# Kernel optimization log

Hardware: AMD Instinct MI355X
Metric: run time of the kernel (lower is better)

Reference implementation:

```python
import jax, jax.numpy as jnp
import numpy as np

HEADS = 56
OUT = 32       # hidden_channels (per-head out dim)
N_FEAT = 128
N_CLASS = 2
N_NODES = 20000
N_EDGES = 100000
N_GRAPHS = 50
EPS_BN = 1e-5


def _gat_conv(x, W, att_src, att_dst, bias, src, dst, n, concat):
    # x: [n, in]; W: [in, H*O]; att_*: [H, O]
    h = (x @ W).reshape(n, HEADS, OUT)                     # [n, H, O]
    a_s = jnp.sum(h * att_src, axis=-1)                    # [n, H]
    a_d = jnp.sum(h * att_dst, axis=-1)                    # [n, H]
    e = jax.nn.leaky_relu(a_s[src] + a_d[dst], 0.2)        # [E, H]
    m = jax.ops.segment_max(e, dst, num_segments=n)        # per-dst max
    ex = jnp.exp(e - m[dst])
    den = jax.ops.segment_sum(ex, dst, num_segments=n)
    alpha = ex / den[dst]                                  # segment softmax over incoming edges
    msg = h[src] * alpha[:, :, None]                       # [E, H, O]
    out = jax.ops.segment_sum(msg, dst, num_segments=n)    # [n, H, O]
    if concat:
        return out.reshape(n, HEADS * OUT) + bias
    return out.mean(axis=1) + bias


def _bn_eval(x, gamma, beta, mean, var):
    return (x - mean) * jax.lax.rsqrt(var + EPS_BN) * gamma + beta


def setup_inputs() -> dict:
    key = jax.random.key(0)
    ks = jax.random.split(key, 20)
    d1 = HEADS * OUT
    inp = {
        'x': jax.random.normal(ks[0], (N_NODES, N_FEAT), jnp.float32),
        'edge_index': jax.random.randint(ks[1], (2, N_EDGES), 0, N_NODES, jnp.int32),
        'batch': jnp.sort(jax.random.randint(ks[2], (N_NODES,), 0, N_GRAPHS, jnp.int32)),
        'W1': jax.random.normal(ks[3], (N_FEAT, d1), jnp.float32) * (1.0 / np.sqrt(N_FEAT)),
        'att_src1': jax.random.normal(ks[4], (HEADS, OUT), jnp.float32) * 0.1,
        'att_dst1': jax.random.normal(ks[5], (HEADS, OUT), jnp.float32) * 0.1,
        'b1': jnp.zeros((d1,), jnp.float32),
        'bn1_g': jnp.ones((d1,), jnp.float32),
        'bn1_b': jnp.zeros((d1,), jnp.float32),
        'bn1_m': jax.random.normal(ks[6], (d1,), jnp.float32) * 0.1,
        'bn1_v': jax.random.uniform(ks[7], (d1,), jnp.float32) + 0.5,
        'W2': jax.random.normal(ks[8], (d1, d1), jnp.float32) * (1.0 / np.sqrt(d1)),
        'att_src2': jax.random.normal(ks[9], (HEADS, OUT), jnp.float32) * 0.1,
        'att_dst2': jax.random.normal(ks[10], (HEADS, OUT), jnp.float32) * 0.1,
        'b2': jnp.zeros((OUT,), jnp.float32),
        'bn2_g': jnp.ones((OUT,), jnp.float32),
        'bn2_b': jnp.zeros((OUT,), jnp.float32),
        'bn2_m': jax.random.normal(ks[11], (OUT,), jnp.float32) * 0.1,
        'bn2_v': jax.random.uniform(ks[12], (OUT,), jnp.float32) + 0.5,
        'lin_w': jax.random.normal(ks[13], (OUT, N_CLASS), jnp.float32) * (1.0 / np.sqrt(OUT)),
        'lin_b': jnp.zeros((N_CLASS,), jnp.float32),
    }
    return inp


def reference(x, edge_index, batch, W1, att_src1, att_dst1, b1, bn1_g, bn1_b, bn1_m, bn1_v,
              W2, att_src2, att_dst2, b2, bn2_g, bn2_b, bn2_m, bn2_v, lin_w, lin_b):
    n = x.shape[0]
    loop = jnp.arange(n, dtype=edge_index.dtype)
    src = jnp.concatenate([edge_index[0], loop])   # PyG GATConv add_self_loops=True
    dst = jnp.concatenate([edge_index[1], loop])

    h = jax.nn.elu(_gat_conv(x, W1, att_src1, att_dst1, b1, src, dst, n, concat=True))
    h = _bn_eval(h, bn1_g, bn1_b, bn1_m, bn1_v)
    # dropout p=0.5 is identity in eval
    h = _gat_conv(h, W2, att_src2, att_dst2, b2, src, dst, n, concat=False)
    h = _bn_eval(h, bn2_g, bn2_b, bn2_m, bn2_v)

    sums = jax.ops.segment_sum(h, batch, num_segments=N_GRAPHS)
    cnt = jax.ops.segment_sum(jnp.ones((n, 1), h.dtype), batch, num_segments=N_GRAPHS)
    pooled = sums / jnp.maximum(cnt, 1.0)          # global_mean_pool
    return pooled @ lin_w + lin_b
```

## Files before the change

kernel.cpp:

```cpp
#include <hip/hip_runtime.h>
#include <hip/hip_bf16.h>
#include <hip/hip_fp8.h>
#include <cstdint>
#include <cstddef>

#define NN     20000
#define NF     128
#define NH     56
#define OC     32
#define DD1    1792
#define NE     100000
#define ETOT   120000
#define NG     50
#define EPS_BN 1e-5f
#define GRP    16
#define EB     16

typedef __bf16 bf16x8 __attribute__((ext_vector_type(8)));
typedef float  floatx4 __attribute__((ext_vector_type(4)));
typedef float  floatx2 __attribute__((ext_vector_type(2)));
typedef unsigned int u32;
typedef __attribute__((address_space(1))) u32 gu32;
typedef __attribute__((address_space(3))) u32 lu32;

__device__ __forceinline__ void async_copy16(void* lds, const void* g) {
    __builtin_amdgcn_global_load_lds((gu32*)const_cast<void*>(g), (lu32*)lds, 16, 0, 0);
}

__device__ __forceinline__ void dec_fp8x4(u32 u, float* v) {
#if __has_builtin(__builtin_amdgcn_cvt_pk_f32_fp8)
    floatx2 lo = __builtin_amdgcn_cvt_pk_f32_fp8(u, false);
    floatx2 hi = __builtin_amdgcn_cvt_pk_f32_fp8(u, true);
    v[0] = lo[0]; v[1] = lo[1]; v[2] = hi[0]; v[3] = hi[1];
#else
    #pragma unroll
    for (int b = 0; b < 4; ++b) {
        __hip_fp8_e4m3 t;
        t.__x = (u >> (8 * b)) & 0xff;
        v[b] = (float)t;
    }
#endif
}

__device__ __forceinline__ void fma_fp8x4(u32 u, float a, float* acc) {
    float v[4];
    dec_fp8x4(u, v);
    #pragma unroll
    for (int b = 0; b < 4; ++b) acc[b] += a * v[b];
}

__global__ __launch_bounds__(256) void cast_bf16_kernel(const float* __restrict__ in,
                                                        __hip_bfloat16* __restrict__ out, int n) {
    int i = blockIdx.x * 256 + threadIdx.x;
    if (i < n) out[i] = __float2bfloat16(in[i]);
}

__global__ __launch_bounds__(256) void transpose_cast_kernel(const float* __restrict__ in,
                                                             __hip_bfloat16* __restrict__ out,
                                                             int R, int C) {
    __shared__ float tile[32][33];
    int c0 = blockIdx.x * 32, r0 = blockIdx.y * 32;
    int tx = threadIdx.x & 31, ty = threadIdx.x >> 5;
    #pragma unroll
    for (int i = 0; i < 32; i += 8) {
        int r = r0 + ty + i, c = c0 + tx;
        if (r < R && c < C) tile[ty + i][tx] = in[(size_t)r * C + c];
    }
    __syncthreads();
    #pragma unroll
    for (int i = 0; i < 32; i += 8) {
        int c = c0 + ty + i, r = r0 + tx;
        if (c < C && r < R) out[(size_t)c * R + r] = __float2bfloat16(tile[tx][ty + i]);
    }
}

__global__ __launch_bounds__(256) void hist_kernel(const int* __restrict__ ei, int* __restrict__ deg) {
    int i = blockIdx.x * 256 + threadIdx.x;
    if (i >= ETOT) return;
    int dst = (i < NE) ? ei[NE + i] : (i - NE);
    atomicAdd(&deg[dst], 1);
}

__global__ __launch_bounds__(1024) void scan_kernel(const int* __restrict__ deg,
                                                    int* __restrict__ rowptr,
                                                    int* __restrict__ cursor) {
    __shared__ int buf[1024];
    int t = threadIdx.x;
    const int CH = (NN + 1023) >> 10;
    int base = t * CH;
    int s = 0;
    for (int j = 0; j < CH; ++j) { int idx = base + j; if (idx < NN) s += deg[idx]; }
    buf[t] = s;
    __syncthreads();
    for (int off = 1; off < 1024; off <<= 1) {
        int v = (t >= off) ? buf[t - off] : 0;
        __syncthreads();
        buf[t] += v;
        __syncthreads();
    }
    int run = buf[t] - s;
    for (int j = 0; j < CH; ++j) {
        int idx = base + j;
        if (idx < NN) { rowptr[idx] = run; cursor[idx] = run; run += deg[idx]; }
    }
    if (t == 1023) rowptr[NN] = buf[1023];
}

__global__ __launch_bounds__(256) void scatter_kernel(const int* __restrict__ ei,
                                                      int* __restrict__ cursor,
                                                      int* __restrict__ csr_src) {
    int i = blockIdx.x * 256 + threadIdx.x;
    if (i >= ETOT) return;
    int s, d;
    if (i < NE) { s = ei[i]; d = ei[NE + i]; } else { s = i - NE; d = i - NE; }
    int pos = atomicAdd(&cursor[d], 1);
    csr_src[pos] = s;
}

__global__ __launch_bounds__(512, 2) void gemm_192(const __hip_bfloat16* __restrict__ A,
                                                   const __hip_bfloat16* __restrict__ Bt,
                                                   unsigned char* __restrict__ C8,
                                                   int M, int N, int K) {
    __shared__ __align__(16) unsigned short lds[2][28672];
    const int tid  = threadIdx.x;
    const int lane = tid & 63, wave = tid >> 6;
    const int wm = wave >> 2, wn = wave & 3;

    const int nbx = N >> 8;
    const int nby = (M + 191) / 192;
    const int nwg = nbx * nby;
    const int q = nwg >> 3, r = nwg & 7;
    const int xcd = blockIdx.x & 7, bidx = blockIdx.x >> 3;
    const int wg = (xcd < r ? xcd * (q + 1) : r * (q + 1) + (xcd - r) * q) + bidx;
    const int by = wg / nbx, bx = wg - by * nbx;
    const int m0 = by * 192, n0 = bx << 8;

    const int NT = K >> 6;

    const int qq = lane >> 4, rr = lane & 15;

    auto stageA = [&](int kt, int b) {
        #pragma unroll
        for (int i = 0; i < 3; ++i) {
            int slot = i * 512 + tid;
            int row = slot >> 3, pch = slot & 7;
            int lc = pch ^ (row & 7);
            int gr = m0 + row; if (gr > M - 1) gr = M - 1;
            async_copy16(&lds[b][slot * 8], A + (size_t)gr * K + (kt << 6) + lc * 8);
        }
    };
    auto stageB = [&](int kt, int b) {
        #pragma unroll
        for (int i = 0; i < 4; ++i) {
            int slot = i * 512 + tid;
            int row = slot >> 3, pch = slot & 7;
            int lc = pch ^ (row & 7);
            async_copy16(&lds[b][12288 + slot * 8], Bt + (size_t)(n0 + row) * K + (kt << 6) + lc * 8);
        }
    };

    floatx4 zero = {0.f, 0.f, 0.f, 0.f};
    floatx4 acc[6][4];
    #pragma unroll
    for (int i = 0; i < 6; ++i)
        #pragma unroll
        for (int jj = 0; jj < 4; ++jj) acc[i][jj] = zero;

    bf16x8 aF[3][2], bA[2][2], bB[2][2];

    auto loadA = [&](int b, int mg) {
        #pragma unroll
        for (int mf = 0; mf < 3; ++mf)
            #pragma unroll
            for (int s = 0; s < 2; ++s) {
                int row = wm * 96 + mg * 48 + mf * 16 + rr;
                int pch = (s * 4 + qq) ^ (row & 7);
                aF[mf][s] = *(const bf16x8*)&lds[b][row * 64 + pch * 8];
            }
    };
    auto loadB = [&](int b, bf16x8 (&bF)[2][2], int ng) {
        #pragma unroll
        for (int nf = 0; nf < 2; ++nf)
            #pragma unroll
            for (int s = 0; s < 2; ++s) {
                int row = wn * 64 + (ng * 2 + nf) * 16 + rr;
                int pch = (s * 4 + qq) ^ (row & 7);
                bF[nf][s] = *(const bf16x8*)&lds[b][12288 + row * 64 + pch * 8];
            }
    };
    auto mfmaQ = [&](int mg, int ng, bf16x8 (&bF)[2][2]) {
        #pragma unroll
        for (int mf = 0; mf < 3; ++mf)
            #pragma unroll
            for (int nf = 0; nf < 2; ++nf)
                #pragma unroll
                for (int s = 0; s < 2; ++s)
                    acc[mg * 3 + mf][ng * 2 + nf] = __builtin_amdgcn_mfma_f32_16x16x32_bf16(
                        aF[mf][s], bF[nf][s], acc[mg * 3 + mf][ng * 2 + nf], 0, 0, 0);
    };

#define SB0 __builtin_amdgcn_sched_barrier(0)
#define GBAR do { SB0; __builtin_amdgcn_s_barrier(); SB0; } while (0)

    stageB(0, 0); stageA(0, 0);
    stageB(1, 1); stageA(1, 1);
    SB0;
    asm volatile("s_waitcnt vmcnt(7)" ::: "memory");
    GBAR;

    for (int t = 0; t < NT; ++t) {
        const int p = t & 1;
        int tp = t + 2; while (tp >= NT) tp -= 2;

        loadA(p, 0); loadB(p, bA, 0);
        GBAR;
        __builtin_amdgcn_s_setprio(1);
        mfmaQ(0, 0, bA);
        __builtin_amdgcn_s_setprio(0);
        GBAR;

        loadB(p, bB, 1);
        stageB(tp, p);
        GBAR;
        __builtin_amdgcn_s_setprio(1);
        mfmaQ(0, 1, bB);
        __builtin_amdgcn_s_setprio(0);
        GBAR;

        loadA(p, 1);
        stageA(tp, p);
        SB0;
        asm volatile("s_waitcnt vmcnt(7)" ::: "memory");
        GBAR;
        __builtin_amdgcn_s_setprio(1);
        mfmaQ(1, 1, bB);
        mfmaQ(1, 0, bA);
        __builtin_amdgcn_s_setprio(0);
        GBAR;
    }
#undef GBAR
#undef SB0

    #pragma unroll
    for (int mt = 0; mt < 6; ++mt) {
        #pragma unroll
        for (int r4 = 0; r4 < 4; ++r4) {
            int rowc = m0 + wm * 96 + mt * 16 + (lane >> 4) * 4 + r4;
            if (rowc < M) {
                float v0 = acc[mt][0][r4], v1 = acc[mt][1][r4];
                float v2 = acc[mt][2][r4], v3 = acc[mt][3][r4];
                unsigned char q8[4];
#if __has_builtin(__builtin_amdgcn_cvt_pk_fp8_f32)
                u32 p01 = (u32)__builtin_amdgcn_cvt_pk_fp8_f32(v0, v1, 0, false);
                u32 p23 = (u32)__builtin_amdgcn_cvt_pk_fp8_f32(v2, v3, 0, false);
                q8[0] = p01 & 0xff; q8[1] = (p01 >> 8) & 0xff;
                q8[2] = p23 & 0xff; q8[3] = (p23 >> 8) & 0xff;
#else
                { __hip_fp8_e4m3 t0(v0), t1(v1), t2(v2), t3(v3);
                  q8[0] = t0.__x; q8[1] = t1.__x; q8[2] = t2.__x; q8[3] = t3.__x; }
#endif
                #pragma unroll
                for (int nt = 0; nt < 4; ++nt) {
                    int col = n0 + wn * 64 + nt * 16 + (lane & 15);
                    C8[(size_t)rowc * N + col] = q8[nt];
                }
            }
        }
    }
}

__global__ __launch_bounds__(256) void attn_score(const unsigned char* __restrict__ h8,
                                                  const float* __restrict__ att_src,
                                                  const float* __restrict__ att_dst,
                                                  float* __restrict__ as_,
                                                  float* __restrict__ ad_) {
    int wave = threadIdx.x >> 6, lane = threadIdx.x & 63;
    int node = blockIdx.x * 4 + wave;
    if (node >= NN || lane >= NH) return;
    const uint2* hp = (const uint2*)(h8 + (size_t)node * DD1 + lane * OC);
    float s = 0.f, d = 0.f;
    #pragma unroll
    for (int jj = 0; jj < 4; ++jj) {
        uint2 u2 = hp[jj];
        u32 us[2] = {u2.x, u2.y};
        #pragma unroll
        for (int w = 0; w < 2; ++w) {
            float v[4];
            dec_fp8x4(us[w], v);
            #pragma unroll
            for (int b = 0; b < 4; ++b) {
                int o = jj * 8 + w * 4 + b;
                s += v[b] * att_src[lane * OC + o];
                d += v[b] * att_dst[lane * OC + o];
            }
        }
    }
    as_[(size_t)node * NH + lane] = s;
    ad_[(size_t)node * NH + lane] = d;
}

template <int LAYER>
__device__ __forceinline__ void flush_node(float* acc, float den, int cur, int f, int lane,
                                           const float* __restrict__ bias,
                                           const float* __restrict__ bng,
                                           const float* __restrict__ bnb,
                                           const float* __restrict__ bnm,
                                           const float* __restrict__ bnv,
                                           void* __restrict__ outp) {
    float inv = 1.f / den;
    #pragma unroll
    for (int k = 0; k < 4; ++k) acc[k] *= inv;

    if constexpr (LAYER == 1) {
        int d0 = f * 256 + lane * 4;
        u32 r01, r23;
        {
            float v0 = acc[0] + bias[d0 + 0];
            float v1 = acc[1] + bias[d0 + 1];
            float v2 = acc[2] + bias[d0 + 2];
            float v3 = acc[3] + bias[d0 + 3];
            v0 = v0 > 0.f ? v0 : expm1f(v0);
            v1 = v1 > 0.f ? v1 : expm1f(v1);
            v2 = v2 > 0.f ? v2 : expm1f(v2);
            v3 = v3 > 0.f ? v3 : expm1f(v3);
            v0 = (v0 - bnm[d0 + 0]) * rsqrtf(bnv[d0 + 0] + EPS_BN) * bng[d0 + 0] + bnb[d0 + 0];
            v1 = (v1 - bnm[d0 + 1]) * rsqrtf(bnv[d0 + 1] + EPS_BN) * bng[d0 + 1] + bnb[d0 + 1];
            v2 = (v2 - bnm[d0 + 2]) * rsqrtf(bnv[d0 + 2] + EPS_BN) * bng[d0 + 2] + bnb[d0 + 2];
            v3 = (v3 - bnm[d0 + 3]) * rsqrtf(bnv[d0 + 3] + EPS_BN) * bng[d0 + 3] + bnb[d0 + 3];
            __hip_bfloat16 b0 = __float2bfloat16(v0), b1 = __float2bfloat16(v1);
            __hip_bfloat16 b2 = __float2bfloat16(v2), b3 = __float2bfloat16(v3);
            r01 = (u32)*(unsigned short*)&b0 | ((u32)*(unsigned short*)&b1 << 16);
            r23 = (u32)*(unsigned short*)&b2 | ((u32)*(unsigned short*)&b3 << 16);
        }
        uint2 pk; pk.x = r01; pk.y = r23;
        *(uint2*)((__hip_bfloat16*)outp + (size_t)cur * DD1 + d0) = pk;
    } else {
        #pragma unroll
        for (int k = 0; k < 4; ++k) {
            acc[k] += __shfl_xor(acc[k], 8, 64);
            acc[k] += __shfl_xor(acc[k], 16, 64);
            acc[k] += __shfl_xor(acc[k], 32, 64);
        }
        if (lane < 8) {
            floatx4 pk;
            #pragma unroll
            for (int k = 0; k < 4; ++k) pk[k] = acc[k] * (1.f / NH);
            *(floatx4*)((float*)outp + ((size_t)cur * 7 + f) * OC + lane * 4) = pk;
        }
    }
    acc[0] = acc[1] = acc[2] = acc[3] = 0.f;
}

template <int LAYER>
__global__ __launch_bounds__(256) void attn_aggregate(const int* __restrict__ rowptr,
                                                      const int* __restrict__ csr_src,
                                                      const float* __restrict__ as_,
                                                      const float* __restrict__ ad_,
                                                      const unsigned char* __restrict__ h8,
                                                      const float* __restrict__ bias,
                                                      const float* __restrict__ bng,
                                                      const float* __restrict__ bnb,
                                                      const float* __restrict__ bnm,
                                                      const float* __restrict__ bnv,
                                                      void* __restrict__ outp) {
    const int wv = threadIdx.x >> 6, lane = threadIdx.x & 63;
    const int w = blockIdx.x * 4 + wv;
    const int NWAVES = 7 * (NN / GRP);
    if (w >= NWAVES) return;
    const int f  = w % 7;
    const int g  = w / 7;
    const int n0 = g * GRP;
    const int off  = f * 256 + lane * 4;
    const int head = f * 8 + (lane >> 3);

    const int e0 = rowptr[n0], e1 = rowptr[n0 + GRP];
    int cur = n0;
    int bound = rowptr[n0 + 1];
    float adv = ad_[(size_t)cur * NH + head];

    float acc[4] = {0.f, 0.f, 0.f, 0.f};
    float m = -1e30f, den = 0.f;

    for (int e = e0; e < e1; e += EB) {
        u32   hv[EB];
        float sv[EB];
        #pragma unroll
        for (int i = 0; i < EB; ++i) {
            int idx = (e + i < e1) ? e + i : e1 - 1;
            int s = csr_src[idx];
            hv[i] = *(const u32*)(h8 + (size_t)s * DD1 + off);
            sv[i] = as_[(size_t)s * NH + head];
        }
        #pragma unroll
        for (int i = 0; i < EB; ++i) {
            if (e + i >= e1) break;
            if (e + i >= bound) {
                flush_node<LAYER>(acc, den, cur, f, lane, bias, bng, bnb, bnm, bnv, outp);
                ++cur;
                bound = rowptr[cur + 1];
                adv = ad_[(size_t)cur * NH + head];
                m = -1e30f; den = 0.f;
            }
            float lr = sv[i] + adv;
            lr = lr > 0.f ? lr : 0.2f * lr;
            float wgt;
            if (lr > m) {
                float scale = __expf(m - lr);
                den = den * scale + 1.f;
                #pragma unroll
                for (int k = 0; k < 4; ++k) acc[k] *= scale;
                m = lr;
                wgt = 1.f;
            } else {
                wgt = __expf(lr - m);
                den += wgt;
            }
            fma_fp8x4(hv[i], wgt, acc);
        }
    }
    flush_node<LAYER>(acc, den, cur, f, lane, bias, bng, bnb, bnm, bnv, outp);
}

__global__ __launch_bounds__(256) void pool_kernel(const float* __restrict__ h2part,
                                                   const int* __restrict__ batch,
                                                   float* __restrict__ sums,
                                                   float* __restrict__ cnt) {
    __shared__ float red[4][OC];
    const int g = blockIdx.x >> 3, c = blockIdx.x & 7;
    const int t = threadIdx.x;
    const int ch = t & 31, nl = t >> 5;
    int lo = 0, hi = NN;
    while (lo < hi) { int mid = (lo + hi) >> 1; if (batch[mid] < g) lo = mid + 1; else hi = mid; }
    const int s = lo;
    hi = NN;
    while (lo < hi) { int mid = (lo + hi) >> 1; if (batch[mid] <= g) lo = mid + 1; else hi = mid; }
    const int e = lo;
    const int len = e - s;
    const int n0 = s + (len * c) / 8;
    const int n1 = s + (len * (c + 1)) / 8;
    float acc = 0.f;
    for (int n = n0 + nl; n < n1; n += 8) {
        const float* p = h2part + (size_t)n * 7 * OC + ch;
        float a = 0.f;
        #pragma unroll
        for (int f = 0; f < 7; ++f) a += p[f * OC];
        acc += a;
    }
    acc += __shfl_xor(acc, 32, 64);
    if ((t & 32) == 0) red[t >> 6][ch] = acc;
    __syncthreads();
    if (t < OC) {
        float total = red[0][t] + red[1][t] + red[2][t] + red[3][t];
        atomicAdd(&sums[g * OC + t], total);
    }
    if (t == 0 && c == 0) cnt[g] = (float)len;
}

__global__ __launch_bounds__(128) void final_kernel(const float* __restrict__ sums,
                                                    const float* __restrict__ cnt,
                                                    const float* __restrict__ b2,
                                                    const float* __restrict__ bn2g,
                                                    const float* __restrict__ bn2b,
                                                    const float* __restrict__ bn2m,
                                                    const float* __restrict__ bn2v,
                                                    const float* __restrict__ lin_w,
                                                    const float* __restrict__ lin_b,
                                                    float* __restrict__ out) {
    int t = threadIdx.x;
    if (t >= NG * 2) return;
    int g = t >> 1, c = t & 1;
    float invc = 1.f / fmaxf(cnt[g], 1.f);
    float acc = lin_b[c];
    #pragma unroll
    for (int o = 0; o < OC; ++o) {
        float pooled = sums[g * OC + o] * invc + b2[o];
        float v = (pooled - bn2m[o]) * rsqrtf(bn2v[o] + EPS_BN) * bn2g[o] + bn2b[o];
        acc += v * lin_w[o * 2 + c];
    }
    out[t] = acc;
}

extern "C" void kernel_launch(void* const* d_in, const int* in_sizes, int n_in,
                              void* d_out, int out_size, void* d_ws, size_t ws_size,
                              hipStream_t stream) {
    const float* x    = (const float*)d_in[0];
    const int*   ei   = (const int*)d_in[1];
    const int*   bat  = (const int*)d_in[2];
    const float* W1   = (const float*)d_in[3];
    const float* at_s1 = (const float*)d_in[4];
    const float* at_d1 = (const float*)d_in[5];
    const float* b1   = (const float*)d_in[6];
    const float* bn1g = (const float*)d_in[7];
    const float* bn1b = (const float*)d_in[8];
    const float* bn1m = (const float*)d_in[9];
    const float* bn1v = (const float*)d_in[10];
    const float* W2   = (const float*)d_in[11];
    const float* at_s2 = (const float*)d_in[12];
    const float* at_d2 = (const float*)d_in[13];
    const float* b2   = (const float*)d_in[14];
    const float* bn2g = (const float*)d_in[15];
    const float* bn2b = (const float*)d_in[16];
    const float* bn2m = (const float*)d_in[17];
    const float* bn2v = (const float*)d_in[18];
    const float* linw = (const float*)d_in[19];
    const float* linb = (const float*)d_in[20];
    float* out = (float*)d_out;

    char* wsp = (char*)d_ws;
    auto alloc = [&](size_t bytes) -> void* {
        void* p = (void*)wsp;
        wsp += (bytes + 255) & ~(size_t)255;
        return p;
    };
    unsigned char*  h8  = (unsigned char*)alloc((size_t)NN * DD1);
    __hip_bfloat16* h1p = (__hip_bfloat16*)alloc((size_t)NN * DD1 * 2);
    __hip_bfloat16* xb  = (__hip_bfloat16*)alloc((size_t)NN * NF * 2);
    __hip_bfloat16* w1t = (__hip_bfloat16*)alloc((size_t)DD1 * NF * 2);
    __hip_bfloat16* w2t = (__hip_bfloat16*)alloc((size_t)DD1 * DD1 * 2);
    float* asb   = (float*)alloc((size_t)NN * NH * 4);
    float* adb   = (float*)alloc((size_t)NN * NH * 4);
    int*   deg   = (int*)alloc((size_t)NN * 4);
    int*   rowp  = (int*)alloc((size_t)(NN + 1) * 4);
    int*   curs  = (int*)alloc((size_t)NN * 4);
    int*   csr   = (int*)alloc((size_t)ETOT * 4);
    float* h2part = (float*)alloc((size_t)NN * 7 * OC * 4);
    float* sums  = (float*)alloc((size_t)(NG * OC + NG) * 4);
    float* cnt   = sums + NG * OC;

    hipMemsetAsync(deg, 0, (size_t)NN * 4, stream);
    hipMemsetAsync(sums, 0, (size_t)(NG * OC + NG) * 4, stream);

    cast_bf16_kernel<<<(NN * NF + 255) / 256, 256, 0, stream>>>(x, xb, NN * NF);
    transpose_cast_kernel<<<dim3(DD1 / 32, NF / 32), 256, 0, stream>>>(W1, w1t, NF, DD1);
    transpose_cast_kernel<<<dim3(DD1 / 32, DD1 / 32), 256, 0, stream>>>(W2, w2t, DD1, DD1);
    hist_kernel<<<(ETOT + 255) / 256, 256, 0, stream>>>(ei, deg);
    scan_kernel<<<1, 1024, 0, stream>>>(deg, rowp, curs);
    scatter_kernel<<<(ETOT + 255) / 256, 256, 0, stream>>>(ei, curs, csr);

    const int AGG_BLOCKS = (7 * (NN / GRP) + 3) / 4;
    const int NBY192 = (NN + 191) / 192;
    const int GEMM_BLOCKS = NBY192 * (DD1 / 256);

    gemm_192<<<GEMM_BLOCKS, 512, 0, stream>>>(xb, w1t, h8, NN, DD1, NF);
    attn_score<<<NN / 4, 256, 0, stream>>>(h8, at_s1, at_d1, asb, adb);
    attn_aggregate<1><<<AGG_BLOCKS, 256, 0, stream>>>(rowp, csr, asb, adb, h8, b1, bn1g, bn1b, bn1m, bn1v, (void*)h1p);

    gemm_192<<<GEMM_BLOCKS, 512, 0, stream>>>(h1p, w2t, h8, NN, DD1, DD1);
    attn_score<<<NN / 4, 256, 0, stream>>>(h8, at_s2, at_d2, asb, adb);
    attn_aggregate<2><<<AGG_BLOCKS, 256, 0, stream>>>(rowp, csr, asb, adb, h8, b2, bn2g, bn2b, bn2m, bn2v, (void*)h2part);

    pool_kernel<<<NG * 8, 256, 0, stream>>>(h2part, bat, sums, cnt);
    final_kernel<<<1, 128, 0, stream>>>(sums, cnt, b2, bn2g, bn2b, bn2m, bn2v, linw, linb, out);
}
```

Baseline: 575.3 us.

## Pack source attention scores beside fp8 features and remap aggregate blocks per XCD

The fp8 feature rows are padded to a 2048-byte stride. Each 256-column chunk gets a 32-byte tail that holds the 8 per-head source attention scores, so the gather in aggregation fetches the features and the score from the same row region. The separate as_ buffer goes away. The aggregate kernel also remaps block IDs so that consecutive logical blocks land on the same XCD, which should improve L2 locality for neighbouring node groups. The cost is a larger h8 buffer and strided GEMM stores.

```diff
diff --git a/kernel.cpp b/kernel.cpp
--- a/kernel.cpp
+++ b/kernel.cpp
@@ -15,6 +15,7 @@
 #define EPS_BN 1e-5f
 #define GRP    16
 #define EB     16
+#define PKROW  2048
 
 typedef __bf16 bf16x8 __attribute__((ext_vector_type(8)));
 typedef float  floatx4 __attribute__((ext_vector_type(4)));
@@ -261,23 +262,23 @@
 #endif
                 #pragma unroll
                 for (int nt = 0; nt < 4; ++nt) {
-                    int col = n0 + wn * 64 + nt * 16 + (lane & 15);
-                    C8[(size_t)rowc * N + col] = q8[nt];
+                    int inner = wn * 64 + nt * 16 + (lane & 15);
+                    C8[(size_t)rowc * PKROW + bx * 288 + inner] = q8[nt];
                 }
             }
         }
     }
 }
 
-__global__ __launch_bounds__(256) void attn_score(const unsigned char* __restrict__ h8,
+__global__ __launch_bounds__(256) void attn_score(unsigned char* __restrict__ h8,
                                                   const float* __restrict__ att_src,
                                                   const float* __restrict__ att_dst,
-                                                  float* __restrict__ as_,
                                                   float* __restrict__ ad_) {
     int wave = threadIdx.x >> 6, lane = threadIdx.x & 63;
     int node = blockIdx.x * 4 + wave;
     if (node >= NN || lane >= NH) return;
-    const uint2* hp = (const uint2*)(h8 + (size_t)node * DD1 + lane * OC);
+    const int f = lane >> 3, j = lane & 7;
+    const uint2* hp = (const uint2*)(h8 + (size_t)node * PKROW + f * 288 + j * 32);
     float s = 0.f, d = 0.f;
     #pragma unroll
     for (int jj = 0; jj < 4; ++jj) {
@@ -295,7 +296,7 @@
             }
         }
     }
-    as_[(size_t)node * NH + lane] = s;
+    *(float*)(h8 + (size_t)node * PKROW + f * 288 + 256 + j * 4) = s;
     ad_[(size_t)node * NH + lane] = d;
 }
 
@@ -354,7 +355,6 @@
 template <int LAYER>
 __global__ __launch_bounds__(256) void attn_aggregate(const int* __restrict__ rowptr,
                                                       const int* __restrict__ csr_src,
-                                                      const float* __restrict__ as_,
                                                       const float* __restrict__ ad_,
                                                       const unsigned char* __restrict__ h8,
                                                       const float* __restrict__ bias,
@@ -362,15 +362,21 @@
                                                       const float* __restrict__ bnb,
                                                       const float* __restrict__ bnm,
                                                       const float* __restrict__ bnv,
-                                                      void* __restrict__ outp) {
+                                                      void* __restrict__ outp,
+                                                      int nblocks) {
+    const int q = nblocks >> 3, r = nblocks & 7;
+    const int xcd = blockIdx.x & 7, bidx = blockIdx.x >> 3;
+    const int bid = (xcd < r ? xcd * (q + 1) : r * (q + 1) + (xcd - r) * q) + bidx;
+
     const int wv = threadIdx.x >> 6, lane = threadIdx.x & 63;
-    const int w = blockIdx.x * 4 + wv;
+    const int w = bid * 4 + wv;
     const int NWAVES = 7 * (NN / GRP);
     if (w >= NWAVES) return;
     const int f  = w % 7;
     const int g  = w / 7;
     const int n0 = g * GRP;
-    const int off  = f * 256 + lane * 4;
+    const int hoff = f * 288 + lane * 4;
+    const int soff = f * 288 + 256 + (lane >> 3) * 4;
     const int head = f * 8 + (lane >> 3);
 
     const int e0 = rowptr[n0], e1 = rowptr[n0 + GRP];
@@ -388,8 +394,9 @@
         for (int i = 0; i < EB; ++i) {
             int idx = (e + i < e1) ? e + i : e1 - 1;
             int s = csr_src[idx];
-            hv[i] = *(const u32*)(h8 + (size_t)s * DD1 + off);
-            sv[i] = as_[(size_t)s * NH + head];
+            const unsigned char* row = h8 + (size_t)s * PKROW;
+            hv[i] = *(const u32*)(row + hoff);
+            sv[i] = *(const float*)(row + soff);
         }
         #pragma unroll
         for (int i = 0; i < EB; ++i) {
@@ -512,12 +519,11 @@
         wsp += (bytes + 255) & ~(size_t)255;
         return p;
     };
-    unsigned char*  h8  = (unsigned char*)alloc((size_t)NN * DD1);
+    unsigned char*  h8  = (unsigned char*)alloc((size_t)NN * PKROW);
     __hip_bfloat16* h1p = (__hip_bfloat16*)alloc((size_t)NN * DD1 * 2);
     __hip_bfloat16* xb  = (__hip_bfloat16*)alloc((size_t)NN * NF * 2);
     __hip_bfloat16* w1t = (__hip_bfloat16*)alloc((size_t)DD1 * NF * 2);
     __hip_bfloat16* w2t = (__hip_bfloat16*)alloc((size_t)DD1 * DD1 * 2);
-    float* asb   = (float*)alloc((size_t)NN * NH * 4);
     float* adb   = (float*)alloc((size_t)NN * NH * 4);
     int*   deg   = (int*)alloc((size_t)NN * 4);
     int*   rowp  = (int*)alloc((size_t)(NN + 1) * 4);
@@ -542,12 +548,12 @@
     const int GEMM_BLOCKS = NBY192 * (DD1 / 256);
 
     gemm_192<<<GEMM_BLOCKS, 512, 0, stream>>>(xb, w1t, h8, NN, DD1, NF);
-    attn_score<<<NN / 4, 256, 0, stream>>>(h8, at_s1, at_d1, asb, adb);
-    attn_aggregate<1><<<AGG_BLOCKS, 256, 0, stream>>>(rowp, csr, asb, adb, h8, b1, bn1g, bn1b, bn1m, bn1v, (void*)h1p);
+    attn_score<<<NN / 4, 256, 0, stream>>>(h8, at_s1, at_d1, adb);
+    attn_aggregate<1><<<AGG_BLOCKS, 256, 0, stream>>>(rowp, csr, adb, h8, b1, bn1g, bn1b, bn1m, bn1v, (void*)h1p, AGG_BLOCKS);
 
     gemm_192<<<GEMM_BLOCKS, 512, 0, stream>>>(h1p, w2t, h8, NN, DD1, DD1);
-    attn_score<<<NN / 4, 256, 0, stream>>>(h8, at_s2, at_d2, asb, adb);
-    attn_aggregate<2><<<AGG_BLOCKS, 256, 0, stream>>>(rowp, csr, asb, adb, h8, b2, bn2g, bn2b, bn2m, bn2v, (void*)h2part);
+    attn_score<<<NN / 4, 256, 0, stream>>>(h8, at_s2, at_d2, adb);
+    attn_aggregate<2><<<AGG_BLOCKS, 256, 0, stream>>>(rowp, csr, adb, h8, b2, bn2g, bn2b, bn2m, bn2v, (void*)h2part, AGG_BLOCKS);
 
     pool_kernel<<<NG * 8, 256, 0, stream>>>(h2part, bat, sums, cnt);
     final_kernel<<<1, 128, 0, stream>>>(sums, cnt, b2, bn2g, bn2b, bn2m, bn2v, linw, linb, out);
```

Measured after the change: 587.7 us. 1.02x slower.
